# Optimization experiments

Measured on AMD Instinct MI355X. Metric: run time of the kernel, lower is better.

Reference implementation:

```python
import jax, jax.numpy as jnp
import numpy as np

CH = 512
GROUPS = 32
EPS = 1e-6


def setup_inputs() -> dict:
    key = jax.random.key(0)
    ks = jax.random.split(key, 12)
    b, c, h, w = 4, CH, 64, 64
    std = 1.0 / np.sqrt(c)
    return {
        "x": jax.random.normal(ks[0], (b, c, h, w), dtype=jnp.float32),
        "norm_gamma": jnp.ones((c,), jnp.float32),
        "norm_beta": jnp.zeros((c,), jnp.float32),
        "wq": jax.random.normal(ks[1], (c, c), jnp.float32) * std,
        "bq": jax.random.normal(ks[2], (c,), jnp.float32) * 0.01,
        "wk": jax.random.normal(ks[3], (c, c), jnp.float32) * std,
        "bk": jax.random.normal(ks[4], (c,), jnp.float32) * 0.01,
        "wv": jax.random.normal(ks[5], (c, c), jnp.float32) * std,
        "bv": jax.random.normal(ks[6], (c,), jnp.float32) * 0.01,
        "wo": jax.random.normal(ks[7], (c, c), jnp.float32) * std,
        "bo": jax.random.normal(ks[8], (c,), jnp.float32) * 0.01,
    }


def _group_norm(x, gamma, beta):
    b, c, h, w = x.shape
    xg = x.reshape(b, GROUPS, c // GROUPS, h, w)
    mean = xg.mean(axis=(2, 3, 4), keepdims=True)
    var = xg.var(axis=(2, 3, 4), keepdims=True)
    xn = ((xg - mean) * jax.lax.rsqrt(var + EPS)).reshape(b, c, h, w)
    return xn * gamma[None, :, None, None] + beta[None, :, None, None]


def reference(x, norm_gamma, norm_beta, wq, bq, wk, bk, wv, bv, wo, bo):
    b, c, h, w = x.shape
    hn = _group_norm(x, norm_gamma, norm_beta)
    hs = hn.reshape(b, c, h * w)  # [b, c, n]
    # 1x1 convs == per-pixel matmuls over channel dim (weight[out,in])
    q = jnp.einsum('oc,bcn->bno', wq, hs) + bq  # [b, n, c]
    k = jnp.einsum('oc,bcn->bon', wk, hs) + bk[None, :, None]  # [b, c, n]
    v = jnp.einsum('oc,bcn->bno', wv, hs) + bv  # [b, n, c]
    scale = c ** (-0.5)
    attn = jax.nn.softmax(jnp.einsum('bnc,bcm->bnm', q, k) * scale, axis=-1)
    out = jnp.einsum('bnm,bmc->bnc', attn, v)  # [b, n, c]
    out = jnp.einsum('oc,bnc->bon', wo, out) + bo[None, :, None]  # [b, c, n]
    return x + out.reshape(b, c, h, w)
```

## Files before the change

kernel.cpp:

```cpp
#include <hip/hip_runtime.h>
#include <hip/hip_bf16.h>
#include <cstdint>

typedef __bf16 bf16;
typedef __bf16 bf16x8 __attribute__((ext_vector_type(8)));
typedef __bf16 bf16x4 __attribute__((ext_vector_type(4)));
typedef float f32x4 __attribute__((ext_vector_type(4)));

__device__ __forceinline__ void gld_lds16(const void* g, void* l) {
  __builtin_amdgcn_global_load_lds((const __attribute__((address_space(1))) void*)g,
                                   (__attribute__((address_space(3))) void*)l, 16, 0, 0);
}

enum { BIAS_NONE = 0, BIAS_COL = 1, BIAS_ROW = 2, BIAS_QK = 3 };
enum { OUT_BF16 = 0, OUT_F32_RESID = 1, OUT_EXP = 2, OUT_VTILED = 3 };

template<int BIAS_MODE, int OUT_MODE>
__global__ __launch_bounds__(256)
void gemm_bt(const bf16* __restrict__ A, long sA, int lda,
             const bf16* __restrict__ Bm, long sB, int ldb,
             void* __restrict__ Cv, long sC, int ldc,
             const float* __restrict__ bias, const float* __restrict__ bias2,
             const float* __restrict__ resid, long sR,
             int K, float scale)
{
  const int bm = blockIdx.x, bn = blockIdx.y, bz = blockIdx.z;
  const char* Ab = (const char*)(A + (long)bz * sA);
  const char* Bb = (const char*)(Bm + (long)bz * sB);
  const int tid = threadIdx.x;
  const int wave = tid >> 6, lane = tid & 63;
  const int wr = wave >> 1, wc = wave & 1;

  __shared__ __attribute__((aligned(128))) char lds[32768];
  char* ldsA = lds;
  char* ldsB = lds + 16384;

  uint32_t aoff[4], boff[4];
#pragma unroll
  for (int i = 0; i < 4; ++i) {
    uint32_t ra = (uint32_t)(wr * 64 + i * 16 + (lane & 15));
    uint32_t la = ra * 128u + (uint32_t)((lane >> 4) << 4);
    aoff[i] = la ^ ((la >> 3) & 0x70u);
    uint32_t rb = (uint32_t)(wc * 64 + i * 16 + (lane & 15));
    uint32_t lb = rb * 128u + (uint32_t)((lane >> 4) << 4);
    boff[i] = lb ^ ((lb >> 3) & 0x70u);
  }
  uint32_t srow[4], sinb[4];
#pragma unroll
  for (int t = 0; t < 4; ++t) {
    uint32_t paddr = (uint32_t)(((wave * 4 + t) * 64 + lane) * 16);
    uint32_t laddr = paddr ^ ((paddr >> 3) & 0x70u);
    srow[t] = laddr >> 7;
    sinb[t] = laddr & 127u;
  }

  const long ldab = (long)lda * 2, ldbb = (long)ldb * 2;
  const long arow0 = (long)bm * 128, brow0 = (long)bn * 128;
  f32x4 acc[4][4] = {};
  const int nK = K >> 6;
  for (int kt = 0; kt < nK; ++kt) {
    const long k0b = (long)kt * 128;
#pragma unroll
    for (int t = 0; t < 4; ++t) {
      gld_lds16(Ab + (arow0 + srow[t]) * ldab + k0b + sinb[t], ldsA + (wave * 4 + t) * 1024);
      gld_lds16(Bb + (brow0 + srow[t]) * ldbb + k0b + sinb[t], ldsB + (wave * 4 + t) * 1024);
    }
    __syncthreads();
#pragma unroll
    for (int kk = 0; kk < 2; ++kk) {
      bf16x8 af[4], bfr[4];
#pragma unroll
      for (int i = 0; i < 4; ++i) {
        af[i]  = *(const bf16x8*)(ldsA + (aoff[i] ^ (kk << 6)));
        bfr[i] = *(const bf16x8*)(ldsB + (boff[i] ^ (kk << 6)));
      }
#pragma unroll
      for (int mi = 0; mi < 4; ++mi)
#pragma unroll
        for (int ni = 0; ni < 4; ++ni)
          acc[mi][ni] = __builtin_amdgcn_mfma_f32_16x16x32_bf16(af[mi], bfr[ni], acc[mi][ni], 0, 0, 0);
    }
    __syncthreads();
  }

  const int cl = lane & 15, rq = lane >> 4;
  const long row0 = (long)bm * 128 + wr * 64;
  const long col0 = (long)bn * 128 + wc * 64;

  if constexpr (OUT_MODE == OUT_F32_RESID) {
    float* Co = (float*)Cv + (long)bz * sC;
    const float* X = resid + (long)bz * sR;
#pragma unroll
    for (int mi = 0; mi < 4; ++mi)
#pragma unroll
      for (int ni = 0; ni < 4; ++ni) {
        const long col = col0 + ni * 16 + cl;
#pragma unroll
        for (int j = 0; j < 4; ++j) {
          const long row = row0 + mi * 16 + rq * 4 + j;
          Co[row * ldc + col] = acc[mi][ni][j] + bias[row] + X[row * ldc + col];
        }
      }
  } else if constexpr (OUT_MODE == OUT_VTILED) {
    bf16* Vt = (bf16*)Cv + (long)bz * sC;
#pragma unroll
    for (int mi = 0; mi < 4; ++mi)
#pragma unroll
      for (int ni = 0; ni < 4; ++ni) {
        const long col = col0 + ni * 16 + cl;
#pragma unroll
        for (int j = 0; j < 4; ++j) {
          const long row = row0 + mi * 16 + rq * 4 + j;
          float v = acc[mi][ni][j] + bias[row];
          Vt[((col >> 3) * 512 + row) * 8 + (col & 7)] = (bf16)v;
        }
      }
  } else if constexpr (BIAS_MODE == BIAS_QK) {
    const bool isq = (col0 < 512);
    bf16* base = (bf16*)Cv + (long)bz * sC + (isq ? 0 : sR);
    const long csub = isq ? 0 : 512;
#pragma unroll
    for (int mi = 0; mi < 4; ++mi)
#pragma unroll
      for (int ni = 0; ni < 4; ++ni) {
        const long col = col0 + ni * 16 + cl;
        const float bc = isq ? bias[col] * scale : bias2[col - 512];
        const float vs = isq ? scale : 1.f;
#pragma unroll
        for (int j = 0; j < 4; ++j) {
          const long row = row0 + mi * 16 + rq * 4 + j;
          base[row * ldc + (col - csub)] = (bf16)(acc[mi][ni][j] * vs + bc);
        }
      }
  } else {
    bf16* Co = (bf16*)Cv + (long)bz * sC;
#pragma unroll
    for (int mi = 0; mi < 4; ++mi)
#pragma unroll
      for (int ni = 0; ni < 4; ++ni) {
        const long col = col0 + ni * 16 + cl;
        float bc = 0.f;
        if (BIAS_MODE == BIAS_COL) bc = bias[col] * scale;
#pragma unroll
        for (int j = 0; j < 4; ++j) {
          const long row = row0 + mi * 16 + rq * 4 + j;
          float v = acc[mi][ni][j] * (BIAS_MODE == BIAS_COL ? scale : 1.f) + bc;
          if (BIAS_MODE == BIAS_ROW) v += bias[row];
          if constexpr (OUT_MODE == OUT_EXP) v = __expf(v);
          Co[row * ldc + col] = (bf16)v;
        }
      }
  }
}

__global__ __launch_bounds__(256, 2)
void gemm_pv11(const bf16* __restrict__ P, long sA,
               const bf16* __restrict__ Vt, long sVt,
               bf16* __restrict__ O, long sC, int swz)
{
  constexpr int T = 64;
  extern __shared__ char lds[];
  char* ldsA = lds;

  int bm, bn, bz;
  if (swz) {
    const int bid = blockIdx.x;
    const int xcd = bid & 7;
    bz = xcd >> 1;
    bn = (bid >> 3) & 1;
    bm = ((bid >> 4) << 1) | (xcd & 1);
  } else { bm = blockIdx.x; bn = blockIdx.y; bz = blockIdx.z; }

  const char* Ab = (const char*)(P + (long)bz * sA) + (long)bm * 64 * 8192;
  const char* Btb = (const char*)(Vt + (long)bz * sVt);
  const int tid = threadIdx.x, wave = tid >> 6, lane = tid & 63;
  const int lg = lane >> 4, l15 = lane & 15;

  const uint32_t ar0 = (uint32_t)(tid >> 3), ac16 = (uint32_t)((tid & 7) * 16);
  const uint32_t aswz = (ar0 & 7) << 4;

  uint32_t aO[4];
#pragma unroll
  for (int mi = 0; mi < 4; ++mi) {
    uint32_t r = (uint32_t)(mi * 16 + l15);
    aO[mi] = r * 128 + (((uint32_t)(lg * 16)) ^ ((r & 7) << 4));
  }
  uint32_t colb[4];
#pragma unroll
  for (int ni = 0; ni < 4; ++ni) {
    uint32_t col = (uint32_t)(bn * 256 + wave * 64 + ni * 16 + l15);
    colb[ni] = col * 16 + (uint32_t)lg * 8192;
  }

  f32x4 acc[4][4] = {};
  float lsum0 = 0.f, lsum1 = 0.f;

  auto loadB = [&](bf16x8 (&b)[4][2], int t) {
#pragma unroll
    for (int ni = 0; ni < 4; ++ni)
#pragma unroll
      for (int kk = 0; kk < 2; ++kk)
        b[ni][kk] = *(const bf16x8*)(Btb + (long)t * 65536 + kk * 32768 + colb[ni]);
  };
  auto loadA0 = [&](int t) -> bf16x8 {
    return *(const bf16x8*)(Ab + (long)ar0 * 8192 + (long)t * 128 + ac16);
  };
  auto loadA1 = [&](int t) -> bf16x8 {
    return *(const bf16x8*)(Ab + (long)(32 + ar0) * 8192 + (long)t * 128 + ac16);
  };
  auto writeA = [&](uint32_t nb, bf16x8 p0, bf16x8 p1) {
#pragma unroll
    for (int j = 0; j < 8; ++j) {
      lsum0 += (float)p0[j];
      lsum1 += (float)p1[j];
    }
    *(bf16x8*)(ldsA + nb * 8192 + ar0 * 128 + (ac16 ^ aswz)) = p0;
    *(bf16x8*)(ldsA + nb * 8192 + (32 + ar0) * 128 + (ac16 ^ aswz)) = p1;
  };

  bf16x8 bE[4][2], bO_[4][2];
  bf16x8 an0, an1;

  loadB(bE, 0);
  an0 = loadA0(0); an1 = loadA1(0);
  writeA(0, an0, an1);
  an0 = loadA0(1); an1 = loadA1(1);
  asm volatile("s_waitcnt lgkmcnt(0)" ::: "memory");
  __builtin_amdgcn_sched_barrier(0);
  __builtin_amdgcn_s_barrier();

  auto body = [&](int t, bf16x8 (&bCur)[4][2], bf16x8 (&bNxt)[4][2]) {
    const uint32_t cur = (uint32_t)(t & 1), nxt = cur ^ 1u;

    if (t + 1 < T) loadB(bNxt, t + 1);
    bf16x8 af[4][2];
#pragma unroll
    for (int mi = 0; mi < 4; ++mi)
#pragma unroll
      for (int kk = 0; kk < 2; ++kk)
        af[mi][kk] = *(const bf16x8*)(ldsA + ((cur * 8192 + aO[mi]) ^ (uint32_t)(kk << 6)));
    if (t + 1 < T) writeA(nxt, an0, an1);
    if (t + 2 < T) { an0 = loadA0(t + 2); an1 = loadA1(t + 2); }

    __builtin_amdgcn_s_setprio(1);
#pragma unroll
    for (int mi = 0; mi < 4; ++mi)
#pragma unroll
      for (int ni = 0; ni < 4; ++ni)
#pragma unroll
        for (int kk = 0; kk < 2; ++kk)
          acc[mi][ni] = __builtin_amdgcn_mfma_f32_16x16x32_bf16(af[mi][kk], bCur[ni][kk], acc[mi][ni], 0, 0, 0);
    __builtin_amdgcn_s_setprio(0);

    if (t + 1 < T) {
      asm volatile("s_waitcnt lgkmcnt(0)" ::: "memory");
      __builtin_amdgcn_sched_barrier(0);
      __builtin_amdgcn_s_barrier();
    }
  };

#pragma unroll 1
  for (int t2 = 0; t2 < T; t2 += 2) {
    body(t2, bE, bO_);
    body(t2 + 1, bO_, bE);
  }

  lsum0 += __shfl_xor(lsum0, 1, 64);
  lsum0 += __shfl_xor(lsum0, 2, 64);
  lsum0 += __shfl_xor(lsum0, 4, 64);
  lsum1 += __shfl_xor(lsum1, 1, 64);
  lsum1 += __shfl_xor(lsum1, 2, 64);
  lsum1 += __shfl_xor(lsum1, 4, 64);
  float* Lrow = (float*)ldsA;
  if ((tid & 7) == 0) {
    Lrow[ar0] = lsum0;
    Lrow[32 + ar0] = lsum1;
  }
  __syncthreads();

  bf16* Co = O + (long)bz * sC + (long)bm * 64 * 512 + (long)bn * 256;
#pragma unroll
  for (int mi = 0; mi < 4; ++mi)
#pragma unroll
    for (int j = 0; j < 4; ++j) {
      const int row = mi * 16 + lg * 4 + j;
      const float invL = 1.f / Lrow[row];
#pragma unroll
      for (int ni = 0; ni < 4; ++ni) {
        const int col = wave * 64 + ni * 16 + l15;
        Co[(long)row * 512 + col] = (bf16)(acc[mi][ni][j] * invL);
      }
    }
}

__global__ __launch_bounds__(256)
void gn_stats(const float* __restrict__ x, float* __restrict__ stats)
{
  const int bg = blockIdx.x;
  const float4* px = (const float4*)(x + (long)bg * 65536);
  float s1 = 0.f, s2 = 0.f;
  for (int i = threadIdx.x; i < 16384; i += 256) {
    float4 f = px[i];
    s1 += f.x + f.y + f.z + f.w;
    s2 += f.x * f.x + f.y * f.y + f.z * f.z + f.w * f.w;
  }
#pragma unroll
  for (int d = 32; d > 0; d >>= 1) {
    s1 += __shfl_xor(s1, d, 64);
    s2 += __shfl_xor(s2, d, 64);
  }
  __shared__ float r1[4], r2[4];
  const int wave = threadIdx.x >> 6, lane = threadIdx.x & 63;
  if (lane == 0) { r1[wave] = s1; r2[wave] = s2; }
  __syncthreads();
  if (threadIdx.x == 0) {
    float t1 = r1[0] + r1[1] + r1[2] + r1[3];
    float t2 = r2[0] + r2[1] + r2[2] + r2[3];
    float mean = t1 * (1.f / 65536.f);
    float var  = t2 * (1.f / 65536.f) - mean * mean;
    stats[bg * 2]     = mean;
    stats[bg * 2 + 1] = rsqrtf(var + 1e-6f);
  }
}

__global__ __launch_bounds__(256)
void gn_apply(const float* __restrict__ x, const float* __restrict__ stats,
              const float* __restrict__ gamma, const float* __restrict__ beta,
              bf16* __restrict__ hn)
{
  const int b = blockIdx.y;
  const int n0 = blockIdx.x * 64;
  __shared__ __attribute__((aligned(16))) char lt[65536];
  const int tid = threadIdx.x;
  for (int i = 0; i < 32; ++i) {
    int f = i * 256 + tid;
    int c = f >> 4;
    int n4 = f & 15;
    float4 xv = *(const float4*)(x + (((long)b * 512 + c) * 4096) + n0 + n4 * 4);
    int g = c >> 4;
    float mean = stats[(b * 32 + g) * 2];
    float rstd = stats[(b * 32 + g) * 2 + 1];
    float ga = gamma[c], be = beta[c];
    float y[4];
    y[0] = (xv.x - mean) * rstd * ga + be;
    y[1] = (xv.y - mean) * rstd * ga + be;
    y[2] = (xv.z - mean) * rstd * ga + be;
    y[3] = (xv.w - mean) * rstd * ga + be;
    uint32_t cb = (uint32_t)(c * 2);
#pragma unroll
    for (int jj = 0; jj < 4; ++jj) {
      uint32_t nl = (uint32_t)(n4 * 4 + jj);
      uint32_t phys = nl * 1024u + (cb ^ (((nl >> 2) & 7u) << 4));
      *(bf16*)(lt + phys) = (bf16)y[jj];
    }
  }
  __syncthreads();
  for (int i = 0; i < 16; ++i) {
    int j = i * 256 + tid;
    uint32_t row = (uint32_t)(j >> 6);
    uint32_t m = (uint32_t)(j & 63);
    uint32_t phys = row * 1024u + ((m * 16u) ^ (((row >> 2) & 7u) << 4));
    uint4 val = *(const uint4*)(lt + phys);
    *(uint4*)((char*)(hn + ((long)b * 4096 + n0 + row) * 512) + m * 16) = val;
  }
}

__global__ __launch_bounds__(256)
void conv_w4(const float* __restrict__ w0, const float* __restrict__ w1,
             const float* __restrict__ w2, const float* __restrict__ w3,
             bf16* __restrict__ dst)
{
  const int z = blockIdx.y;
  const float* src = (z == 0) ? w0 : (z == 1) ? w1 : (z == 2) ? w2 : w3;
  const int i = blockIdx.x * 256 + threadIdx.x;
  float4 f = ((const float4*)src)[i];
  bf16x4 o;
  o[0] = (bf16)f.x; o[1] = (bf16)f.y; o[2] = (bf16)f.z; o[3] = (bf16)f.w;
  ((bf16x4*)(dst))[(long)z * 65536 + i] = o;
}

extern "C" void kernel_launch(void* const* d_in, const int* in_sizes, int n_in,
                              void* d_out, int out_size, void* d_ws, size_t ws_size,
                              hipStream_t stream)
{
  const float* x     = (const float*)d_in[0];
  const float* gamma = (const float*)d_in[1];
  const float* beta  = (const float*)d_in[2];
  const float* wq = (const float*)d_in[3];
  const float* bq = (const float*)d_in[4];
  const float* wk = (const float*)d_in[5];
  const float* bk = (const float*)d_in[6];
  const float* wv = (const float*)d_in[7];
  const float* bv = (const float*)d_in[8];
  const float* wo = (const float*)d_in[9];
  const float* bo = (const float*)d_in[10];
  float* out = (float*)d_out;

  char* ws = (char*)d_ws;
  bf16* hn  = (bf16*)(ws + 0);
  bf16* q   = (bf16*)(ws + 16777216);
  bf16* k   = (bf16*)(ws + 33554432);
  bf16* v   = (bf16*)(ws + 50331648);
  bf16* O   = (bf16*)(ws + 67108864);
  bf16* wqb = (bf16*)(ws + 83886080);
  bf16* wvb = (bf16*)(ws + 84934656);
  bf16* wob = (bf16*)(ws + 85458944);
  float* gstats = (float*)(ws + 85983232);
  bf16* S   = (bf16*)(ws + 85984256);

  const long sBC = 2097152;
  const long sS1 = 16777216;
  const long K_OFS = 8388608;
  const float scale = 0.044194173824159216f;

  const int LDS_PV = 16384;
  hipFuncSetAttribute(reinterpret_cast<const void*>(gemm_pv11),
                      hipFuncAttributeMaxDynamicSharedMemorySize, LDS_PV);

  conv_w4<<<dim3(256, 4), 256, 0, stream>>>(wq, wk, wv, wo, wqb);
  gn_stats<<<128, 256, 0, stream>>>(x, gstats);
  gn_apply<<<dim3(64, 4), 256, 0, stream>>>(x, gstats, gamma, beta, hn);

  gemm_bt<BIAS_QK, OUT_BF16><<<dim3(32, 8, 4), 256, 0, stream>>>(
      hn, sBC, 512, wqb, 0, 512, q, sBC, 512,
      bq, bk, nullptr, K_OFS, 512, scale);
  gemm_bt<BIAS_ROW, OUT_VTILED><<<dim3(4, 32, 4), 256, 0, stream>>>(
      wvb, 0, 512, hn, sBC, 512, v, sBC, 4096,
      bv, nullptr, nullptr, 0, 512, 1.f);

  const bool tier1 = ws_size >= (size_t)220202112;
  if (tier1) {
    gemm_bt<BIAS_NONE, OUT_EXP><<<dim3(32, 32, 4), 256, 0, stream>>>(
        q, sBC, 512, k, sBC, 512, S, sS1, 4096,
        nullptr, nullptr, nullptr, 0, 512, 1.f);
    gemm_pv11<<<dim3(512, 1, 1), 256, LDS_PV, stream>>>(
        S, sS1, v, sBC, O, sBC, 1);
  } else {
    for (int b = 0; b < 4; ++b) {
      gemm_bt<BIAS_NONE, OUT_EXP><<<dim3(32, 32, 1), 256, 0, stream>>>(
          q + b * sBC, 0, 512, k + b * sBC, 0, 512, S, 0, 4096,
          nullptr, nullptr, nullptr, 0, 512, 1.f);
      gemm_pv11<<<dim3(64, 2, 1), 256, LDS_PV, stream>>>(
          S, 0, v + b * sBC, 0, O + b * sBC, 0, 0);
    }
  }

  gemm_bt<BIAS_ROW, OUT_F32_RESID><<<dim3(4, 32, 4), 256, 0, stream>>>(
      wob, 0, 512, O, sBC, 512, out, sBC, 4096,
      bo, nullptr, x, sBC, 512, 1.f);
}
```

Measured before the change: 264.5 us.

## Store Q/K in k-tiled layout and use LDS-free register-direct QK^T GEMM

```diff
diff --git a/kernel.cpp b/kernel.cpp
--- a/kernel.cpp
+++ b/kernel.cpp
@@ -124,12 +124,13 @@
 #pragma unroll
       for (int ni = 0; ni < 4; ++ni) {
         const long col = col0 + ni * 16 + cl;
-        const float bc = isq ? bias[col] * scale : bias2[col - 512];
+        const long c = col - csub;
+        const float bc = isq ? bias[col] * scale : bias2[c];
         const float vs = isq ? scale : 1.f;
 #pragma unroll
         for (int j = 0; j < 4; ++j) {
           const long row = row0 + mi * 16 + rq * 4 + j;
-          base[row * ldc + (col - csub)] = (bf16)(acc[mi][ni][j] * vs + bc);
+          base[((c >> 3) * 4096 + row) * 8 + (c & 7)] = (bf16)(acc[mi][ni][j] * vs + bc);
         }
       }
   } else {
@@ -151,6 +152,88 @@
         }
       }
   }
+}
+
+__global__ __launch_bounds__(256, 2)
+void gemm_s12(const bf16* __restrict__ Qt, long sQ,
+              const bf16* __restrict__ Kt, long sK,
+              bf16* __restrict__ S, long sS)
+{
+  constexpr int T = 8;
+  const int bm = blockIdx.x, bn = blockIdx.y, bz = blockIdx.z;
+  const char* Qb = (const char*)(Qt + (long)bz * sQ);
+  const char* Kb = (const char*)(Kt + (long)bz * sK);
+  const int tid = threadIdx.x, wave = tid >> 6, lane = tid & 63;
+  const int wr = wave >> 1, wc = wave & 1;
+  const int lg = lane >> 4, l15 = lane & 15;
+
+  long aOff[4], bOff[4];
+#pragma unroll
+  for (int mi = 0; mi < 4; ++mi) {
+    long row = (long)bm * 128 + wr * 64 + mi * 16 + l15;
+    aOff[mi] = (long)lg * 65536 + row * 16;
+  }
+#pragma unroll
+  for (int ni = 0; ni < 4; ++ni) {
+    long row = (long)bn * 128 + wc * 64 + ni * 16 + l15;
+    bOff[ni] = (long)lg * 65536 + row * 16;
+  }
+
+  f32x4 acc[4][4] = {};
+
+  auto loadA = [&](bf16x8 (&a)[4][2], int t) {
+#pragma unroll
+    for (int mi = 0; mi < 4; ++mi)
+#pragma unroll
+      for (int kk = 0; kk < 2; ++kk)
+        a[mi][kk] = *(const bf16x8*)(Qb + (long)t * 524288 + kk * 262144 + aOff[mi]);
+  };
+  auto loadB = [&](bf16x8 (&b)[4][2], int t) {
+#pragma unroll
+    for (int ni = 0; ni < 4; ++ni)
+#pragma unroll
+      for (int kk = 0; kk < 2; ++kk)
+        b[ni][kk] = *(const bf16x8*)(Kb + (long)t * 524288 + kk * 262144 + bOff[ni]);
+  };
+
+  bf16x8 aE[4][2], bE[4][2], aO_[4][2], bO_[4][2];
+  loadA(aE, 0); loadB(bE, 0);
+
+  auto body = [&](int t, bf16x8 (&aC)[4][2], bf16x8 (&bC)[4][2],
+                  bf16x8 (&aN)[4][2], bf16x8 (&bN)[4][2]) {
+    if (t + 1 < T) { loadA(aN, t + 1); loadB(bN, t + 1); }
+    __builtin_amdgcn_s_setprio(1);
+#pragma unroll
+    for (int mi = 0; mi < 4; ++mi)
+#pragma unroll
+      for (int ni = 0; ni < 4; ++ni)
+#pragma unroll
+        for (int kk = 0; kk < 2; ++kk)
+          acc[mi][ni] = __builtin_amdgcn_mfma_f32_16x16x32_bf16(aC[mi][kk], bC[ni][kk], acc[mi][ni], 0, 0, 0);
+    __builtin_amdgcn_s_setprio(0);
+  };
+
+#pragma unroll 1
+  for (int t2 = 0; t2 < T; t2 += 2) {
+    body(t2, aE, bE, aO_, bO_);
+    body(t2 + 1, aO_, bO_, aE, bE);
+  }
+
+  const int cl = l15, rq = lg;
+  const long row0 = (long)bm * 128 + wr * 64;
+  const long col0 = (long)bn * 128 + wc * 64;
+  bf16* Co = S + (long)bz * sS;
+#pragma unroll
+  for (int mi = 0; mi < 4; ++mi)
+#pragma unroll
+    for (int ni = 0; ni < 4; ++ni) {
+      const long col = col0 + ni * 16 + cl;
+#pragma unroll
+      for (int j = 0; j < 4; ++j) {
+        const long row = row0 + mi * 16 + rq * 4 + j;
+        Co[row * 4096 + col] = (bf16)__expf(acc[mi][ni][j]);
+      }
+    }
 }
 
 __global__ __launch_bounds__(256, 2)
@@ -430,16 +513,13 @@
 
   const bool tier1 = ws_size >= (size_t)220202112;
   if (tier1) {
-    gemm_bt<BIAS_NONE, OUT_EXP><<<dim3(32, 32, 4), 256, 0, stream>>>(
-        q, sBC, 512, k, sBC, 512, S, sS1, 4096,
-        nullptr, nullptr, nullptr, 0, 512, 1.f);
+    gemm_s12<<<dim3(32, 32, 4), 256, 0, stream>>>(q, sBC, k, sBC, S, sS1);
     gemm_pv11<<<dim3(512, 1, 1), 256, LDS_PV, stream>>>(
         S, sS1, v, sBC, O, sBC, 1);
   } else {
     for (int b = 0; b < 4; ++b) {
-      gemm_bt<BIAS_NONE, OUT_EXP><<<dim3(32, 32, 1), 256, 0, stream>>>(
-          q + b * sBC, 0, 512, k + b * sBC, 0, 512, S, 0, 4096,
-          nullptr, nullptr, nullptr, 0, 512, 1.f);
+      gemm_s12<<<dim3(32, 32, 1), 256, 0, stream>>>(
+          q + b * sBC, 0, k + b * sBC, 0, S, 0);
       gemm_pv11<<<dim3(64, 2, 1), 256, LDS_PV, stream>>>(
           S, 0, v + b * sBC, 0, O + b * sBC, 0, 0);
     }
```

After: 272.4 us. 3.0% more time.
